# Optimization experiments

Hardware: AMD Instinct MI355X
Metric: run time of the kernel (lower is better)

Reference implementation:

```python
import jax, jax.numpy as jnp
import numpy as np

LUT_DIM = 33  # classic 3D color LUT grid size


def apply_lut(LUT, img):
    """Trilinear 3D-LUT apply. LUT: [3, D, D, D] (indexed [c, b, g, r]); img: [3, H, W] in ~[0,1]."""
    D = LUT.shape[1]
    x = img * (D - 1)                                   # [3, H, W] continuous grid coords
    i0 = jnp.clip(jnp.floor(x).astype(jnp.int32), 0, D - 2)
    f = x - i0.astype(x.dtype)                          # fractional offsets
    r0, g0, b0 = i0[0], i0[1], i0[2]                    # [H, W] int indices per channel
    fr, fg, fb = f[0], f[1], f[2]

    def corner(db, dg, dr):
        # 8-corner gather: [3, H, W]
        return LUT[:, b0 + db, g0 + dg, r0 + dr]

    w000 = (1 - fb) * (1 - fg) * (1 - fr)
    w001 = (1 - fb) * (1 - fg) * fr
    w010 = (1 - fb) * fg * (1 - fr)
    w011 = (1 - fb) * fg * fr
    w100 = fb * (1 - fg) * (1 - fr)
    w101 = fb * (1 - fg) * fr
    w110 = fb * fg * (1 - fr)
    w111 = fb * fg * fr

    out = (w000 * corner(0, 0, 0) + w001 * corner(0, 0, 1)
           + w010 * corner(0, 1, 0) + w011 * corner(0, 1, 1)
           + w100 * corner(1, 0, 0) + w101 * corner(1, 0, 1)
           + w110 * corner(1, 1, 0) + w111 * corner(1, 1, 1))
    return out


def setup_inputs() -> dict:
    key = jax.random.key(0)
    k1, k2, k3, k4 = jax.random.split(key, 4)
    H, W, N = 2160, 3840, 350
    gt = jax.random.uniform(k1, (3, H, W), dtype=jnp.float32)
    # Scale LUT entries by 1/N so the unweighted sum of 350 LUTs stays in ~[0,1]
    # (keeps the second apply_lut's gather indices in-range, as a real identity-ish LUT stack would).
    lut = jax.random.uniform(k2, (2, N, 3, LUT_DIM, LUT_DIM, LUT_DIM), dtype=jnp.float32) / N
    L0 = jax.random.normal(k3, (N,), dtype=jnp.float32)
    L1 = jax.random.normal(k4, (N,), dtype=jnp.float32)
    return {"gt": gt, "lut": lut, "L0": L0, "L1": L1}


def reference(gt, lut, L0, L1):
    # NOTE: the original forward computes softmax(L0)/softmax(L1) but never uses
    # the weights: it sums the LUT slices unweighted. We reproduce that faithfully;
    # the softmaxes are dead code and omitted.
    CL0 = lut[0].sum(axis=0)          # [3, D, D, D]
    I_s = apply_lut(CL0, gt)          # [3, H, W]
    CL1 = lut[1].sum(axis=0)          # [3, D, D, D]
    I_f = apply_lut(CL1, I_s)         # [3, H, W]
    return I_f
```

## Files before the change

### kernel.cpp

```cpp
#include <hip/hip_runtime.h>

#define HW_PIX (2160 * 3840)
#define QPIX   (HW_PIX / 4)
#define D   33
#define D2  (33 * 33)
#define D3  (33 * 33 * 33)
#define M   (3 * D3)
#define NLUT 350
#define TWO_M (2 * M)

#define PIDX  (32 * 32 * 32)
#define PU4   (PIDX * 2)

#define HB     422

typedef float        f4 __attribute__((ext_vector_type(4)));
typedef unsigned int u4 __attribute__((ext_vector_type(4)));

template<int NS>
__global__ __launch_bounds__(256) void reduce_kernel(
    const float* __restrict__ lut,
    float* __restrict__ accum)
{
    const int lane = threadIdx.x & 63;
    const int w    = threadIdx.x >> 6;
    const int bid  = blockIdx.x;
    const int s    = bid / (2 * HB);
    const int rem  = bid - s * (2 * HB);
    const int h    = rem / HB;
    const int vb   = (rem - h * HB) * 256;

    const int C = NLUT / NS;
    const int q = C >> 2, r = C & 3;
    const int start = s * C + w * q + min(w, r);
    const int count = q + (w < r ? 1 : 0);

    const float* __restrict__ hb =
        lut + ((long long)h * NLUT + start) * M;

    int off[4];
    #pragma unroll
    for (int k = 0; k < 4; ++k) {
        int v = vb + lane + 64 * k;
        off[k] = (v < M) ? v : 0;
    }

    float s0 = 0.f, s1 = 0.f, s2 = 0.f, s3 = 0.f;
    const float* p = hb;
    #pragma unroll 4
    for (int n = 0; n < count; ++n, p += M) {
        s0 += p[off[0]];
        s1 += p[off[1]];
        s2 += p[off[2]];
        s3 += p[off[3]];
    }

    __shared__ float red[4][64][4];
    red[w][lane][0] = s0;
    red[w][lane][1] = s1;
    red[w][lane][2] = s2;
    red[w][lane][3] = s3;
    __syncthreads();

    const int o = threadIdx.x;
    const int v = vb + o;
    if (v < M) {
        int ln = o & 63, k = o >> 6;
        float t = (red[0][ln][k] + red[1][ln][k])
                + (red[2][ln][k] + red[3][ln][k]);
        accum[((long long)(s * 2 + h)) * M + v] = t;
    }
}

__global__ __launch_bounds__(256) void pack_kernel(
    const float* __restrict__ accum,
    uint4* __restrict__ packed,
    int ns)
{
    int t = blockIdx.x * 256 + threadIdx.x;
    if (t >= 2 * PIDX) return;
    int h = t >> 15;
    int e = t & (PIDX - 1);
    int b = e >> 10;
    int g = (e >> 5) & 31;
    int r = e & 31;

    const float* A = accum + (long long)h * M;
    uint4 E[2];
    #pragma unroll
    for (int bb = 0; bb < 2; ++bb) {
        unsigned q[12];
        int j = 0;
        #pragma unroll
        for (int gg = 0; gg < 2; ++gg)
            #pragma unroll
            for (int rr = 0; rr < 2; ++rr)
                #pragma unroll
                for (int c = 0; c < 3; ++c) {
                    int i = c * D3 + ((b + bb) * D + (g + gg)) * D + (r + rr);
                    float v = A[i];
                    for (int s = 1; s < ns; ++s) v += A[i + (long long)s * TWO_M];
                    v = fminf(fmaxf(v, 0.0f), 1.0f);
                    q[j++] = (unsigned)(v * 1023.0f + 0.5f);
                }
        E[bb].x = q[0] | (q[1]  << 10) | (q[2]  << 20);
        E[bb].y = q[3] | (q[4]  << 10) | (q[5]  << 20);
        E[bb].z = q[6] | (q[7]  << 10) | (q[8]  << 20);
        E[bb].w = q[9] | (q[10] << 10) | (q[11] << 20);
    }
    packed[2 * t]     = E[0];
    packed[2 * t + 1] = E[1];
}

__device__ __forceinline__ void apply4(const u4* __restrict__ L,
                                       const float* r, const float* g, const float* b,
                                       float* pr, float* pg, float* pb)
{
    u4 E0[4], E1[4];
    float fr[4], fg[4], fb[4];
    #pragma unroll
    for (int i = 0; i < 4; ++i) {
        float xr = r[i] * 32.0f, xg = g[i] * 32.0f, xb = b[i] * 32.0f;
        int r0 = min(max((int)xr, 0), 31);
        int g0 = min(max((int)xg, 0), 31);
        int b0 = min(max((int)xb, 0), 31);
        fr[i] = xr - (float)r0;
        fg[i] = xg - (float)g0;
        fb[i] = xb - (float)b0;
        int idx = (b0 << 10) + (g0 << 5) + r0;
        E0[i] = L[2 * idx];
        E1[i] = L[2 * idx + 1];
    }
    const float inv = 1.0f / 1023.0f;
    #pragma unroll
    for (int i = 0; i < 4; ++i) {
        float w00 = (1.0f - fg[i]) * (1.0f - fr[i]);
        float w01 = (1.0f - fg[i]) * fr[i];
        float w10 = fg[i] * (1.0f - fr[i]);
        float w11 = fg[i] * fr[i];
        float wb0 = 1.0f - fb[i], wb1 = fb[i];

        float sr, sg, sb;
        {
            float a00 = wb0 * w00, a01 = wb0 * w01, a10 = wb0 * w10, a11 = wb0 * w11;
            sr = a00 * (float)( E0[i].x        & 1023) + a01 * (float)( E0[i].y        & 1023)
               + a10 * (float)( E0[i].z        & 1023) + a11 * (float)( E0[i].w        & 1023);
            sg = a00 * (float)((E0[i].x >> 10) & 1023) + a01 * (float)((E0[i].y >> 10) & 1023)
               + a10 * (float)((E0[i].z >> 10) & 1023) + a11 * (float)((E0[i].w >> 10) & 1023);
            sb = a00 * (float)((E0[i].x >> 20) & 1023) + a01 * (float)((E0[i].y >> 20) & 1023)
               + a10 * (float)((E0[i].z >> 20) & 1023) + a11 * (float)((E0[i].w >> 20) & 1023);
        }
        {
            float a00 = wb1 * w00, a01 = wb1 * w01, a10 = wb1 * w10, a11 = wb1 * w11;
            sr += a00 * (float)( E1[i].x        & 1023) + a01 * (float)( E1[i].y        & 1023)
                + a10 * (float)( E1[i].z        & 1023) + a11 * (float)( E1[i].w        & 1023);
            sg += a00 * (float)((E1[i].x >> 10) & 1023) + a01 * (float)((E1[i].y >> 10) & 1023)
                + a10 * (float)((E1[i].z >> 10) & 1023) + a11 * (float)((E1[i].w >> 10) & 1023);
            sb += a00 * (float)((E1[i].x >> 20) & 1023) + a01 * (float)((E1[i].y >> 20) & 1023)
                + a10 * (float)((E1[i].z >> 20) & 1023) + a11 * (float)((E1[i].w >> 20) & 1023);
        }
        pr[i] = sr * inv; pg[i] = sg * inv; pb[i] = sb * inv;
    }
}

__global__ __launch_bounds__(256) void fused_apply_kernel(
    const float* __restrict__ gt,
    const u4* __restrict__ packed,
    float* __restrict__ out)
{
    int q = blockIdx.x * 256 + threadIdx.x;
    if (q >= QPIX) return;

    const f4* g4 = (const f4*)gt;
    f4 Rv = __builtin_nontemporal_load(g4 + q);
    f4 Gv = __builtin_nontemporal_load(g4 + q + QPIX);
    f4 Bv = __builtin_nontemporal_load(g4 + q + 2 * QPIX);

    float r0[4] = {Rv.x, Rv.y, Rv.z, Rv.w};
    float g0[4] = {Gv.x, Gv.y, Gv.z, Gv.w};
    float b0[4] = {Bv.x, Bv.y, Bv.z, Bv.w};
    float r1[4], g1[4], b1[4], r2[4], g2[4], b2[4];

    apply4(packed,       r0, g0, b0, r1, g1, b1);
    apply4(packed + PU4, r1, g1, b1, r2, g2, b2);

    f4 Ro = {r2[0], r2[1], r2[2], r2[3]};
    f4 Go = {g2[0], g2[1], g2[2], g2[3]};
    f4 Bo = {b2[0], b2[1], b2[2], b2[3]};
    f4* o4 = (f4*)out;
    __builtin_nontemporal_store(Ro, o4 + q);
    __builtin_nontemporal_store(Go, o4 + q + QPIX);
    __builtin_nontemporal_store(Bo, o4 + q + 2 * QPIX);
}

extern "C" void kernel_launch(void* const* d_in, const int* in_sizes, int n_in,
                              void* d_out, int out_size, void* d_ws, size_t ws_size,
                              hipStream_t stream)
{
    const float* gt  = (const float*)d_in[0];
    const float* lut = (const float*)d_in[1];
    float* out = (float*)d_out;

    const size_t packed_bytes = (size_t)2 * PIDX * 2 * sizeof(uint4);

    size_t a2 = ((size_t)2 * TWO_M * sizeof(float) + 31) & ~(size_t)31;
    size_t a1 = ((size_t)1 * TWO_M * sizeof(float) + 31) & ~(size_t)31;
    int ns; size_t poff;
    if (ws_size >= a2 + packed_bytes) { ns = 2; poff = a2; }
    else                              { ns = 1; poff = a1; }

    float* accum  = (float*)d_ws;
    u4*    packed = (u4*)((char*)d_ws + poff);

    if (ns == 2)
        reduce_kernel<2><<<dim3(2 * 2 * HB), dim3(256), 0, stream>>>(lut, accum);
    else
        reduce_kernel<1><<<dim3(1 * 2 * HB), dim3(256), 0, stream>>>(lut, accum);

    pack_kernel<<<dim3((2 * PIDX + 255) / 256), dim3(256), 0, stream>>>(
        accum, (uint4*)packed, ns);
    fused_apply_kernel<<<dim3((QPIX + 255) / 256), dim3(256), 0, stream>>>(gt, packed, out);
}
```

Baseline: 555.2 us.

## Fuse reduce, pack and apply into one cooperative persistent kernel with grid syncs

Replaces the three separate launches with a single cooperative kernel of 1024 blocks. It reduces the 350 LUTs in 4 splits using float4 loads over 1024-element tiles, then packs the LUTs, then applies them over pixels in a grid-stride loop, with grid.sync between stages. A three-launch path remains as a fallback if the cooperative launch fails or the workspace is too small. This is meant to remove launch gaps and tail effects between stages. In exchange it adds grid-wide barriers and caps parallelism in the apply stage at 1024 persistent blocks.

```diff
diff --git a/kernel.cpp b/kernel.cpp
--- a/kernel.cpp
+++ b/kernel.cpp
@@ -1,91 +1,77 @@
 #include <hip/hip_runtime.h>
+#include <hip/hip_cooperative_groups.h>
+
+namespace cg = cooperative_groups;
 
 #define HW_PIX (2160 * 3840)
 #define QPIX   (HW_PIX / 4)
 #define D   33
-#define D2  (33 * 33)
 #define D3  (33 * 33 * 33)
 #define M   (3 * D3)
+#define MP  107812
 #define NLUT 350
-#define TWO_M (2 * M)
 
 #define PIDX  (32 * 32 * 32)
 #define PU4   (PIDX * 2)
 
-#define HB     422
-
-typedef float        f4 __attribute__((ext_vector_type(4)));
-typedef unsigned int u4 __attribute__((ext_vector_type(4)));
-
-template<int NS>
-__global__ __launch_bounds__(256) void reduce_kernel(
-    const float* __restrict__ lut,
-    float* __restrict__ accum)
-{
-    const int lane = threadIdx.x & 63;
-    const int w    = threadIdx.x >> 6;
-    const int bid  = blockIdx.x;
-    const int s    = bid / (2 * HB);
-    const int rem  = bid - s * (2 * HB);
-    const int h    = rem / HB;
-    const int vb   = (rem - h * HB) * 256;
-
-    const int C = NLUT / NS;
-    const int q = C >> 2, r = C & 3;
-    const int start = s * C + w * q + min(w, r);
-    const int count = q + (w < r ? 1 : 0);
-
-    const float* __restrict__ hb =
-        lut + ((long long)h * NLUT + start) * M;
-
-    int off[4];
-    #pragma unroll
-    for (int k = 0; k < 4; ++k) {
-        int v = vb + lane + 64 * k;
-        off[k] = (v < M) ? v : 0;
-    }
-
-    float s0 = 0.f, s1 = 0.f, s2 = 0.f, s3 = 0.f;
-    const float* p = hb;
-    #pragma unroll 4
-    for (int n = 0; n < count; ++n, p += M) {
-        s0 += p[off[0]];
-        s1 += p[off[1]];
-        s2 += p[off[2]];
-        s3 += p[off[3]];
-    }
-
-    __shared__ float red[4][64][4];
-    red[w][lane][0] = s0;
-    red[w][lane][1] = s1;
-    red[w][lane][2] = s2;
-    red[w][lane][3] = s3;
-    __syncthreads();
-
-    const int o = threadIdx.x;
-    const int v = vb + o;
-    if (v < M) {
-        int ln = o & 63, k = o >> 6;
-        float t = (red[0][ln][k] + red[1][ln][k])
-                + (red[2][ln][k] + red[3][ln][k]);
-        accum[((long long)(s * 2 + h)) * M + v] = t;
-    }
-}
-
-__global__ __launch_bounds__(256) void pack_kernel(
-    const float* __restrict__ accum,
-    uint4* __restrict__ packed,
-    int ns)
-{
-    int t = blockIdx.x * 256 + threadIdx.x;
-    if (t >= 2 * PIDX) return;
-    int h = t >> 15;
-    int e = t & (PIDX - 1);
-    int b = e >> 10;
-    int g = (e >> 5) & 31;
-    int r = e & 31;
-
-    const float* A = accum + (long long)h * M;
+#define CH    1024
+#define HT    ((M + CH - 1) / CH)
+#define NSMAX 4
+
+#define NB    1024
+#define BLK   256
+#define NT    (NB * BLK)
+
+typedef float        f4  __attribute__((ext_vector_type(4)));
+typedef unsigned int u4  __attribute__((ext_vector_type(4)));
+typedef float        f4u __attribute__((ext_vector_type(4), aligned(4)));
+
+__device__ __forceinline__ void reduce_tile(const float* __restrict__ lut,
+                                            float* __restrict__ accum,
+                                            int tile, int ns)
+{
+    const int s  = tile / (2 * HT);
+    const int rm = tile - s * (2 * HT);
+    const int h  = rm / HT;
+    const int ti = rm - h * HT;
+    const int vb = ti * CH;
+
+    const int cbase = NLUT / ns, crem = NLUT % ns;
+    const int start = s * cbase + min(s, crem);
+    const int count = cbase + (s < crem ? 1 : 0);
+
+    const float* __restrict__ base = lut + ((long long)h * NLUT + start) * M;
+    float* __restrict__ arow = accum + (long long)(s * 2 + h) * MP;
+
+    if (vb + CH <= M) {
+        const int idx = vb + ((threadIdx.x >> 6) << 8) + ((threadIdx.x & 63) << 2);
+        const float* p = base + idx;
+        f4 a = {0.f, 0.f, 0.f, 0.f};
+        #pragma unroll 4
+        for (int n = 0; n < count; ++n, p += M)
+            a += *(const f4u*)p;
+        *(f4*)(arow + idx) = a;
+    } else {
+        for (int e = vb + (int)threadIdx.x; e < M; e += BLK) {
+            const float* p = base + e;
+            float a = 0.f;
+            for (int n = 0; n < count; ++n, p += M) a += *p;
+            arow[e] = a;
+        }
+    }
+}
+
+__device__ __forceinline__ void pack_entry(const float* __restrict__ accum,
+                                           uint4* __restrict__ packed,
+                                           int t, int ns)
+{
+    const int h = t >> 15;
+    const int e = t & (PIDX - 1);
+    const int b = e >> 10;
+    const int g = (e >> 5) & 31;
+    const int r = e & 31;
+
+    const float* A = accum + (long long)h * MP;
     uint4 E[2];
     #pragma unroll
     for (int bb = 0; bb < 2; ++bb) {
@@ -98,8 +84,8 @@
                 #pragma unroll
                 for (int c = 0; c < 3; ++c) {
                     int i = c * D3 + ((b + bb) * D + (g + gg)) * D + (r + rr);
-                    float v = A[i];
-                    for (int s = 1; s < ns; ++s) v += A[i + (long long)s * TWO_M];
+                    float v = 0.f;
+                    for (int s = 0; s < ns; ++s) v += A[i + (long long)s * 2 * MP];
                     v = fminf(fmaxf(v, 0.0f), 1.0f);
                     q[j++] = (unsigned)(v * 1023.0f + 0.5f);
                 }
@@ -163,14 +149,10 @@
     }
 }
 
-__global__ __launch_bounds__(256) void fused_apply_kernel(
-    const float* __restrict__ gt,
-    const u4* __restrict__ packed,
-    float* __restrict__ out)
-{
-    int q = blockIdx.x * 256 + threadIdx.x;
-    if (q >= QPIX) return;
-
+__device__ __forceinline__ void apply_quad(const float* __restrict__ gt,
+                                           const u4* __restrict__ packed,
+                                           float* __restrict__ out, int q)
+{
     const f4* g4 = (const f4*)gt;
     f4 Rv = __builtin_nontemporal_load(g4 + q);
     f4 Gv = __builtin_nontemporal_load(g4 + q + QPIX);
@@ -193,6 +175,52 @@
     __builtin_nontemporal_store(Bo, o4 + q + 2 * QPIX);
 }
 
+__global__ __launch_bounds__(BLK, 4) void pipeline_kernel(
+    const float* __restrict__ gt,
+    const float* __restrict__ lut,
+    float* __restrict__ accum,
+    u4* __restrict__ packed,
+    float* __restrict__ out)
+{
+    cg::grid_group grid = cg::this_grid();
+    const int bid = blockIdx.x;
+
+    if (bid < NSMAX * 2 * HT)
+        reduce_tile(lut, accum, bid, NSMAX);
+    grid.sync();
+
+    {
+        int t = bid * BLK + (int)threadIdx.x;
+        if (t < 2 * PIDX)
+            pack_entry(accum, (uint4*)packed, t, NSMAX);
+    }
+    grid.sync();
+
+    for (int q = bid * BLK + (int)threadIdx.x; q < QPIX; q += NT)
+        apply_quad(gt, packed, out, q);
+}
+
+__global__ __launch_bounds__(BLK) void reduce_fb(const float* __restrict__ lut,
+                                                 float* __restrict__ accum)
+{
+    if (blockIdx.x < 2 * HT) reduce_tile(lut, accum, blockIdx.x, 1);
+}
+
+__global__ __launch_bounds__(BLK) void pack_fb(const float* __restrict__ accum,
+                                               uint4* __restrict__ packed)
+{
+    int t = blockIdx.x * BLK + (int)threadIdx.x;
+    if (t < 2 * PIDX) pack_entry(accum, packed, t, 1);
+}
+
+__global__ __launch_bounds__(BLK) void apply_fb(const float* __restrict__ gt,
+                                                const u4* __restrict__ packed,
+                                                float* __restrict__ out)
+{
+    int q = blockIdx.x * BLK + (int)threadIdx.x;
+    if (q < QPIX) apply_quad(gt, packed, out, q);
+}
+
 extern "C" void kernel_launch(void* const* d_in, const int* in_sizes, int n_in,
                               void* d_out, int out_size, void* d_ws, size_t ws_size,
                               hipStream_t stream)
@@ -201,23 +229,23 @@
     const float* lut = (const float*)d_in[1];
     float* out = (float*)d_out;
 
-    const size_t packed_bytes = (size_t)2 * PIDX * 2 * sizeof(uint4);
-
-    size_t a2 = ((size_t)2 * TWO_M * sizeof(float) + 31) & ~(size_t)31;
-    size_t a1 = ((size_t)1 * TWO_M * sizeof(float) + 31) & ~(size_t)31;
-    int ns; size_t poff;
-    if (ws_size >= a2 + packed_bytes) { ns = 2; poff = a2; }
-    else                              { ns = 1; poff = a1; }
-
-    float* accum  = (float*)d_ws;
-    u4*    packed = (u4*)((char*)d_ws + poff);
-
-    if (ns == 2)
-        reduce_kernel<2><<<dim3(2 * 2 * HB), dim3(256), 0, stream>>>(lut, accum);
-    else
-        reduce_kernel<1><<<dim3(1 * 2 * HB), dim3(256), 0, stream>>>(lut, accum);
-
-    pack_kernel<<<dim3((2 * PIDX + 255) / 256), dim3(256), 0, stream>>>(
-        accum, (uint4*)packed, ns);
-    fused_apply_kernel<<<dim3((QPIX + 255) / 256), dim3(256), 0, stream>>>(gt, packed, out);
-}
+    const size_t packed_bytes = (size_t)2 * PU4 * sizeof(uint4);
+    const size_t a4 = (((size_t)NSMAX * 2 * MP * sizeof(float)) + 31) & ~(size_t)31;
+    const size_t a1 = (((size_t)1     * 2 * MP * sizeof(float)) + 31) & ~(size_t)31;
+
+    hipError_t e = hipErrorUnknown;
+    if (ws_size >= a4 + packed_bytes) {
+        float* accum  = (float*)d_ws;
+        u4*    packed = (u4*)((char*)d_ws + a4);
+        void* args[] = {(void*)&gt, (void*)&lut, (void*)&accum, (void*)&packed, (void*)&out};
+        e = hipLaunchCooperativeKernel((const void*)pipeline_kernel,
+                                       dim3(NB), dim3(BLK), args, 0, stream);
+    }
+    if (e != hipSuccess) {
+        float* accum  = (float*)d_ws;
+        u4*    packed = (u4*)((char*)d_ws + a1);
+        reduce_fb<<<dim3(2 * HT), dim3(BLK), 0, stream>>>(lut, accum);
+        pack_fb<<<dim3((2 * PIDX + BLK - 1) / BLK), dim3(BLK), 0, stream>>>(accum, (uint4*)packed);
+        apply_fb<<<dim3((QPIX + BLK - 1) / BLK), dim3(BLK), 0, stream>>>(gt, packed, out);
+    }
+}
```

Result: slower. 790.0 us (+42.3%).

## Restructure LUT reduction with vectorized nontemporal loads and 8-way LUT split

Applied to the files above, without the earlier changes.

Rewrites the LUT-stack reduction so each thread sums a float4 column across its share of LUTs, using two independent accumulator streams and nontemporal loads. The work is split 8 ways over the LUT dimension instead of 2, with a padded row stride so partial sums stay aligned. The pack kernel then adds 8 partials per element. This aims to raise memory-level parallelism on the roughly 200 MB LUT read, at the cost of more workspace and more partial-sum traffic in the pack step.

```diff
diff --git a/kernel.cpp b/kernel.cpp
--- a/kernel.cpp
+++ b/kernel.cpp
@@ -3,72 +3,64 @@
 #define HW_PIX (2160 * 3840)
 #define QPIX   (HW_PIX / 4)
 #define D   33
-#define D2  (33 * 33)
 #define D3  (33 * 33 * 33)
 #define M   (3 * D3)
+#define MP  107812
 #define NLUT 350
-#define TWO_M (2 * M)
 
 #define PIDX  (32 * 32 * 32)
 #define PU4   (PIDX * 2)
 
-#define HB     422
-
-typedef float        f4 __attribute__((ext_vector_type(4)));
-typedef unsigned int u4 __attribute__((ext_vector_type(4)));
+#define CH    1024
+#define HT    ((M + CH - 1) / CH)
+
+typedef float        f4  __attribute__((ext_vector_type(4)));
+typedef unsigned int u4  __attribute__((ext_vector_type(4)));
+typedef float        f4u __attribute__((ext_vector_type(4), aligned(4)));
 
 template<int NS>
 __global__ __launch_bounds__(256) void reduce_kernel(
     const float* __restrict__ lut,
     float* __restrict__ accum)
 {
-    const int lane = threadIdx.x & 63;
-    const int w    = threadIdx.x >> 6;
-    const int bid  = blockIdx.x;
-    const int s    = bid / (2 * HB);
-    const int rem  = bid - s * (2 * HB);
-    const int h    = rem / HB;
-    const int vb   = (rem - h * HB) * 256;
-
-    const int C = NLUT / NS;
-    const int q = C >> 2, r = C & 3;
-    const int start = s * C + w * q + min(w, r);
-    const int count = q + (w < r ? 1 : 0);
-
-    const float* __restrict__ hb =
-        lut + ((long long)h * NLUT + start) * M;
-
-    int off[4];
-    #pragma unroll
-    for (int k = 0; k < 4; ++k) {
-        int v = vb + lane + 64 * k;
-        off[k] = (v < M) ? v : 0;
-    }
-
-    float s0 = 0.f, s1 = 0.f, s2 = 0.f, s3 = 0.f;
-    const float* p = hb;
-    #pragma unroll 4
-    for (int n = 0; n < count; ++n, p += M) {
-        s0 += p[off[0]];
-        s1 += p[off[1]];
-        s2 += p[off[2]];
-        s3 += p[off[3]];
-    }
-
-    __shared__ float red[4][64][4];
-    red[w][lane][0] = s0;
-    red[w][lane][1] = s1;
-    red[w][lane][2] = s2;
-    red[w][lane][3] = s3;
-    __syncthreads();
-
-    const int o = threadIdx.x;
-    const int v = vb + o;
-    if (v < M) {
-        int ln = o & 63, k = o >> 6;
-        float t = (red[0][ln][k] + red[1][ln][k])
-                + (red[2][ln][k] + red[3][ln][k]);
-        accum[((long long)(s * 2 + h)) * M + v] = t;
+    const int bid = blockIdx.x;
+    const int s   = bid / (2 * HT);
+    const int rm  = bid - s * (2 * HT);
+    const int h   = rm / HT;
+    const int ti  = rm - h * HT;
+    const int vb  = ti * CH;
+
+    const int cbase = NLUT / NS, crem = NLUT % NS;
+    const int start = s * cbase + min(s, crem);
+    const int count = cbase + (s < crem ? 1 : 0);
+
+    const float* __restrict__ base = lut + ((long long)h * NLUT + start) * M;
+    float* __restrict__ arow = accum + (long long)(s * 2 + h) * MP;
+
+    if (vb + CH <= M) {
+        const int idx = vb + (int)threadIdx.x * 4;
+        const int c0  = count >> 1;
+        f4 a = {0.f, 0.f, 0.f, 0.f};
+        f4 b = {0.f, 0.f, 0.f, 0.f};
+        const float* pA = base + idx;
+        const float* pB = base + (long long)c0 * M + idx;
+        #pragma unroll 2
+        for (int n = 0; n < c0; ++n, pA += M, pB += M) {
+            a += __builtin_nontemporal_load((const f4u*)pA);
+            b += __builtin_nontemporal_load((const f4u*)pB);
+        }
+        if (count & 1)
+            b += __builtin_nontemporal_load((const f4u*)pB);
+        a += b;
+        *(f4*)(arow + idx) = a;
+    } else {
+        for (int e = vb + (int)threadIdx.x; e < M; e += 256) {
+            const float* p = base + e;
+            float a = 0.f;
+            for (int n = 0; n < count; ++n, p += M)
+                a += __builtin_nontemporal_load(p);
+            arow[e] = a;
+        }
     }
 }
 
@@ -85,7 +77,7 @@
     int g = (e >> 5) & 31;
     int r = e & 31;
 
-    const float* A = accum + (long long)h * M;
+    const float* A = accum + (long long)h * MP;
     uint4 E[2];
     #pragma unroll
     for (int bb = 0; bb < 2; ++bb) {
@@ -98,8 +90,9 @@
                 #pragma unroll
                 for (int c = 0; c < 3; ++c) {
                     int i = c * D3 + ((b + bb) * D + (g + gg)) * D + (r + rr);
-                    float v = A[i];
-                    for (int s = 1; s < ns; ++s) v += A[i + (long long)s * TWO_M];
+                    float v = 0.f;
+                    for (int s = 0; s < ns; ++s)
+                        v += A[i + (long long)s * 2 * MP];
                     v = fminf(fmaxf(v, 0.0f), 1.0f);
                     q[j++] = (unsigned)(v * 1023.0f + 0.5f);
                 }
@@ -201,21 +194,21 @@
     const float* lut = (const float*)d_in[1];
     float* out = (float*)d_out;
 
-    const size_t packed_bytes = (size_t)2 * PIDX * 2 * sizeof(uint4);
-
-    size_t a2 = ((size_t)2 * TWO_M * sizeof(float) + 31) & ~(size_t)31;
-    size_t a1 = ((size_t)1 * TWO_M * sizeof(float) + 31) & ~(size_t)31;
+    const size_t packed_bytes = (size_t)2 * PU4 * sizeof(uint4);
+    const size_t a8 = (((size_t)8 * 2 * MP * sizeof(float)) + 31) & ~(size_t)31;
+    const size_t a1 = (((size_t)1 * 2 * MP * sizeof(float)) + 31) & ~(size_t)31;
+
     int ns; size_t poff;
-    if (ws_size >= a2 + packed_bytes) { ns = 2; poff = a2; }
+    if (ws_size >= a8 + packed_bytes) { ns = 8; poff = a8; }
     else                              { ns = 1; poff = a1; }
 
     float* accum  = (float*)d_ws;
     u4*    packed = (u4*)((char*)d_ws + poff);
 
-    if (ns == 2)
-        reduce_kernel<2><<<dim3(2 * 2 * HB), dim3(256), 0, stream>>>(lut, accum);
+    if (ns == 8)
+        reduce_kernel<8><<<dim3(8 * 2 * HT), dim3(256), 0, stream>>>(lut, accum);
     else
-        reduce_kernel<1><<<dim3(1 * 2 * HB), dim3(256), 0, stream>>>(lut, accum);
+        reduce_kernel<1><<<dim3(1 * 2 * HT), dim3(256), 0, stream>>>(lut, accum);
 
     pack_kernel<<<dim3((2 * PIDX + 255) / 256), dim3(256), 0, stream>>>(
         accum, (uint4*)packed, ns);
```

Result: slower. 580.2 us (+4.5%).
